# Kernel optimization log

Measured on AMD Instinct MI355X. Metric: run time of the kernel, lower is better.

The kernel has to match this reference:

```python
import jax, jax.numpy as jnp
import numpy as np

B, S, D, H = 4, 2048, 1024, 16
DK = D // H


def setup_inputs() -> dict:
    key = jax.random.key(0)
    ks = jax.random.split(key, 12)
    s = 1.0 / np.sqrt(D)
    return {
        "query": jax.random.normal(ks[0], (B, S, D), jnp.float32),
        "key": jax.random.normal(ks[1], (B, S, D), jnp.float32),
        "value": jax.random.normal(ks[2], (B, S, D), jnp.float32),
        "attention_mask": jax.random.randint(ks[3], (B, S, S), 0, 2, jnp.int32),
        "w_q": jax.random.uniform(ks[4], (D, D), jnp.float32, -s, s),
        "b_q": jax.random.uniform(ks[5], (D,), jnp.float32, -s, s),
        "w_k": jax.random.uniform(ks[6], (D, D), jnp.float32, -s, s),
        "b_k": jax.random.uniform(ks[7], (D,), jnp.float32, -s, s),
        "w_v": jax.random.uniform(ks[8], (D, D), jnp.float32, -s, s),
        "b_v": jax.random.uniform(ks[9], (D,), jnp.float32, -s, s),
        "w_o": jax.random.uniform(ks[10], (D, D), jnp.float32, -s, s),
        "b_o": jax.random.uniform(ks[11], (D,), jnp.float32, -s, s),
    }


def reference(query, key, value, attention_mask, w_q, b_q, w_k, b_k, w_v, b_v, w_o, b_o):
    # project and split heads: [B,S,D] -> [B,H,S,DK]
    def proj(x, w, b):
        y = jnp.einsum('bsd,ed->bse', x, w) + b  # torch Linear: x @ W.T + b
        return y.reshape(B, S, H, DK).transpose(0, 2, 1, 3)

    q = proj(query, w_q, b_q)
    k = proj(key, w_k, b_k)
    v = proj(value, w_v, b_v)

    scores = jnp.einsum('bhqd,bhkd->bhqk', q, k) / np.sqrt(DK).astype(np.float32)
    mask = attention_mask[:, None, :, :]  # broadcast over heads
    scores = jnp.where(mask == 0, jnp.float32(-1e9), scores)
    attn = jax.nn.softmax(scores, axis=-1)  # dropout is identity in eval
    out = jnp.einsum('bhqk,bhkd->bhqd', attn, v)
    out = out.transpose(0, 2, 1, 3).reshape(B, S, D)
    return jnp.einsum('bsd,ed->bse', out, w_o) + b_o
```

## Files before the change

### kernel.cpp

```cpp
#include <hip/hip_runtime.h>


#define B_ 4
#define S_ 2048
#define D_ 1024
#define H_ 16
#define DK_ 64
#define M_ (B_ * S_)

typedef __attribute__((ext_vector_type(4))) float f32x4;
typedef __attribute__((ext_vector_type(8))) short s16x8;
typedef __attribute__((ext_vector_type(8))) unsigned short u16x8;
typedef __attribute__((ext_vector_type(4))) unsigned short u16x4;

__device__ __forceinline__ unsigned short f2bf(float f) {
    union { float f; unsigned int u; } v; v.f = f;
    unsigned int u = v.u;
    return (unsigned short)((u + 0x7FFFu + ((u >> 16) & 1u)) >> 16);
}

__device__ __forceinline__ void gl2lds16(const unsigned short* g, unsigned short* l) {
    __builtin_amdgcn_global_load_lds((const __attribute__((address_space(1))) void*)g,
                                     (__attribute__((address_space(3))) void*)l, 16, 0, 0);
}

__global__ __launch_bounds__(256) void cvt_bf16(const float* __restrict__ x,
                                                unsigned short* __restrict__ y, int n) {
    int i = (blockIdx.x * 256 + threadIdx.x) * 8;
    if (i + 8 <= n) {
        float4 a = *(const float4*)(x + i);
        float4 b = *(const float4*)(x + i + 4);
        u16x8 r;
        r[0] = f2bf(a.x); r[1] = f2bf(a.y); r[2] = f2bf(a.z); r[3] = f2bf(a.w);
        r[4] = f2bf(b.x); r[5] = f2bf(b.y); r[6] = f2bf(b.z); r[7] = f2bf(b.w);
        *(u16x8*)(y + i) = r;
    }
}

__global__ __launch_bounds__(256) void pack_mask(const int* __restrict__ m,
                                                 unsigned long long* __restrict__ pm) {
    int t = blockIdx.x * 256 + threadIdx.x;
    unsigned long long bits = __ballot(m[t] != 0);
    if ((threadIdx.x & 63) == 0) pm[t >> 6] = bits;
}

template <int MODE>
__global__ __launch_bounds__(256) void gemm_bt(const unsigned short* __restrict__ A,
                                               const unsigned short* __restrict__ Bt,
                                               const float* __restrict__ bias,
                                               float scale, void* __restrict__ Y) {
    __shared__ __align__(16) unsigned short As[128 * 64];
    __shared__ __align__(16) unsigned short Bs[128 * 64];
    const int tid = threadIdx.x;
    const int wave = tid >> 6, lane = tid & 63, quad = lane >> 4, l16 = lane & 15;
    const int m0 = blockIdx.x * 128, n0 = blockIdx.y * 128;
    const int rw = (wave & 1) * 64, cw = (wave >> 1) * 64;

    const int srow = tid >> 3, scol = (tid & 7) * 8;
    const unsigned short* ga = A + (size_t)(m0 + srow) * 1024 + scol;
    const unsigned short* gb = Bt + (size_t)(n0 + srow) * 1024 + scol;

    f32x4 acc[4][4];
#pragma unroll
    for (int mi = 0; mi < 4; mi++)
#pragma unroll
        for (int ni = 0; ni < 4; ni++) acc[mi][ni] = (f32x4){0.f, 0.f, 0.f, 0.f};

    for (int k0 = 0; k0 < 1024; k0 += 64) {
#pragma unroll
        for (int r = 0; r < 4; r++) {
            gl2lds16(ga + (size_t)(r * 32) * 1024 + k0, &As[(r * 256 + tid) * 8]);
            gl2lds16(gb + (size_t)(r * 32) * 1024 + k0, &Bs[(r * 256 + tid) * 8]);
        }
        __syncthreads();
#pragma unroll
        for (int kk = 0; kk < 64; kk += 32) {
            s16x8 af[4], bf[4];
#pragma unroll
            for (int mi = 0; mi < 4; mi++)
                af[mi] = *(const s16x8*)&As[(rw + mi * 16 + l16) * 64 + kk + quad * 8];
#pragma unroll
            for (int ni = 0; ni < 4; ni++)
                bf[ni] = *(const s16x8*)&Bs[(cw + ni * 16 + l16) * 64 + kk + quad * 8];
#pragma unroll
            for (int mi = 0; mi < 4; mi++)
#pragma unroll
                for (int ni = 0; ni < 4; ni++)
                    acc[mi][ni] = __builtin_amdgcn_mfma_f32_16x16x32_bf16(af[mi], bf[ni], acc[mi][ni], 0, 0, 0);
        }
        __syncthreads();
    }

    float bv[4];
#pragma unroll
    for (int ni = 0; ni < 4; ni++) bv[ni] = bias[n0 + cw + ni * 16 + l16];
#pragma unroll
    for (int mi = 0; mi < 4; mi++) {
        const int rb = m0 + rw + mi * 16 + quad * 4;
        const int b = rb >> 11, s0 = rb & 2047;
#pragma unroll
        for (int ni = 0; ni < 4; ni++) {
            const int col = n0 + cw + ni * 16 + l16;
            if (MODE == 3) {
#pragma unroll
                for (int i = 0; i < 4; i++)
                    ((float*)Y)[(size_t)(rb + i) * 1024 + col] = (acc[mi][ni][i] + bv[ni]) * scale;
            } else {
                const int h = col >> 6, dk = col & 63;
                if (MODE == 1) {
#pragma unroll
                    for (int i = 0; i < 4; i++)
                        ((unsigned short*)Y)[((size_t)(b * H_ + h) * S_ + s0 + i) * DK_ + dk] =
                            f2bf((acc[mi][ni][i] + bv[ni]) * scale);
                } else {
                    u16x4 pk;
#pragma unroll
                    for (int i = 0; i < 4; i++) pk[i] = f2bf((acc[mi][ni][i] + bv[ni]) * scale);
                    *(u16x4*)&((unsigned short*)Y)[((size_t)(b * H_ + h) * DK_ + dk) * S_ + s0] = pk;
                }
            }
        }
    }
}

__global__ __launch_bounds__(256) void attn_kernel(const unsigned short* __restrict__ Q,
                                                   const unsigned short* __restrict__ K,
                                                   const unsigned short* __restrict__ Vt,
                                                   const unsigned long long* __restrict__ pm,
                                                   unsigned short* __restrict__ ctx) {
    __shared__ __align__(16) unsigned short Ks[64 * 72];
    __shared__ __align__(16) unsigned short Vs[64 * 72];
    __shared__ __align__(16) unsigned short Ps[4 * 16 * 72];

    const int tid = threadIdx.x;
    const int wave = tid >> 6, lane = tid & 63, quad = lane >> 4, l16 = lane & 15;
    const int bh = blockIdx.y, b = bh >> 4, h = bh & 15;
    const int q0 = blockIdx.x * 64;
    const int lr = tid >> 2, lc = (tid & 3) * 16;

    const unsigned short* Kbase = K + (size_t)bh * S_ * DK_;
    const unsigned short* Vbase = Vt + (size_t)bh * DK_ * S_;
    const unsigned long long* pmb = pm + (size_t)b * S_ * 32;

    s16x8 qf0, qf1;
    {
        const unsigned short* qr = Q + ((size_t)bh * S_ + q0 + wave * 16 + l16) * DK_ + quad * 8;
        qf0 = *(const s16x8*)qr;
        qf1 = *(const s16x8*)(qr + 32);
    }

    f32x4 oacc[4];
    float lpart[4];
#pragma unroll
    for (int ct = 0; ct < 4; ct++) oacc[ct] = (f32x4){0.f, 0.f, 0.f, 0.f};
#pragma unroll
    for (int i = 0; i < 4; i++) lpart[i] = 0.f;

    unsigned short* pw = &Ps[wave * 16 * 72];
    const int shl0 = 31 - l16;
    const int shl1 = 15 - l16;

    for (int kt = 0; kt < S_ / 64; kt++) {
        const int k0 = kt * 64;
        const unsigned short* gk = Kbase + (size_t)(k0 + lr) * DK_ + lc;
        const unsigned short* gv = Vbase + (size_t)lr * S_ + k0 + lc;
        *(uint4*)&Ks[lr * 72 + lc] = *(const uint4*)gk;
        *(uint4*)&Ks[lr * 72 + lc + 8] = *(const uint4*)(gk + 8);
        *(uint4*)&Vs[lr * 72 + lc] = *(const uint4*)gv;
        *(uint4*)&Vs[lr * 72 + lc + 8] = *(const uint4*)(gv + 8);
        __syncthreads();

        f32x4 sacc[4];
#pragma unroll
        for (int ct = 0; ct < 4; ct++) sacc[ct] = (f32x4){0.f, 0.f, 0.f, 0.f};
#pragma unroll
        for (int kk = 0; kk < 64; kk += 32) {
            s16x8 af = kk ? qf1 : qf0;
#pragma unroll
            for (int ct = 0; ct < 4; ct++) {
                s16x8 bf = *(const s16x8*)&Ks[(ct * 16 + l16) * 72 + kk + quad * 8];
                sacc[ct] = __builtin_amdgcn_mfma_f32_16x16x32_bf16(af, bf, sacc[ct], 0, 0, 0);
            }
        }

#pragma unroll
        for (int i = 0; i < 4; i++) {
            const int qg = q0 + wave * 16 + quad * 4 + i;
            const uint2 mv = *(const uint2*)&pmb[(size_t)qg * 32 + kt];
#pragma unroll
            for (int ct = 0; ct < 4; ct++) {
                const unsigned mm = (ct & 2) ? mv.y : mv.x;
                const int sh = (ct & 1) ? shl1 : shl0;
                const float sv = ((int)(mm << sh) < 0) ? sacc[ct][i] : -1e30f;
                const float p = exp2f(sv);
                lpart[i] += p;
                pw[(quad * 4 + i) * 72 + ct * 16 + l16] = f2bf(p);
            }
        }

#pragma unroll
        for (int kk = 0; kk < 64; kk += 32) {
            s16x8 af = *(const s16x8*)&pw[l16 * 72 + kk + quad * 8];
#pragma unroll
            for (int ct = 0; ct < 4; ct++) {
                s16x8 bf = *(const s16x8*)&Vs[(ct * 16 + l16) * 72 + kk + quad * 8];
                oacc[ct] = __builtin_amdgcn_mfma_f32_16x16x32_bf16(af, bf, oacc[ct], 0, 0, 0);
            }
        }
        __syncthreads();
    }

    float rl[4];
#pragma unroll
    for (int i = 0; i < 4; i++) {
        float l = lpart[i];
#pragma unroll
        for (int off = 1; off <= 8; off <<= 1) l += __shfl_xor(l, off);
        rl[i] = 1.0f / l;
    }
#pragma unroll
    for (int ct = 0; ct < 4; ct++) {
        const int col = h * DK_ + ct * 16 + l16;
#pragma unroll
        for (int i = 0; i < 4; i++) {
            const int sg = q0 + wave * 16 + quad * 4 + i;
            ctx[((size_t)(b * S_ + sg)) * D_ + col] = f2bf(oacc[ct][i] * rl[i]);
        }
    }
}

extern "C" void kernel_launch(void* const* d_in, const int* in_sizes, int n_in,
                              void* d_out, int out_size, void* d_ws, size_t ws_size,
                              hipStream_t stream) {
    const float* query = (const float*)d_in[0];
    const float* key   = (const float*)d_in[1];
    const float* value = (const float*)d_in[2];
    const int*   mask  = (const int*)d_in[3];
    const float* w_q = (const float*)d_in[4];
    const float* b_q = (const float*)d_in[5];
    const float* w_k = (const float*)d_in[6];
    const float* b_k = (const float*)d_in[7];
    const float* w_v = (const float*)d_in[8];
    const float* b_v = (const float*)d_in[9];
    const float* w_o = (const float*)d_in[10];
    const float* b_o = (const float*)d_in[11];

    char* ws = (char*)d_ws;
    const size_t XSZ = (size_t)M_ * D_ * 2;
    const size_t WSZ = (size_t)D_ * D_ * 2;
    unsigned short* Xq  = (unsigned short*)(ws);
    unsigned short* Xk  = (unsigned short*)(ws + XSZ);
    unsigned short* Xv  = (unsigned short*)(ws + 2 * XSZ);
    unsigned short* Wq  = (unsigned short*)(ws + 3 * XSZ);
    unsigned short* Wk  = (unsigned short*)(ws + 3 * XSZ + WSZ);
    unsigned short* Wv  = (unsigned short*)(ws + 3 * XSZ + 2 * WSZ);
    unsigned short* Wo  = (unsigned short*)(ws + 3 * XSZ + 3 * WSZ);
    unsigned short* Qb  = (unsigned short*)(ws + 3 * XSZ + 4 * WSZ);
    unsigned short* Kb  = (unsigned short*)(ws + 4 * XSZ + 4 * WSZ);
    unsigned short* Vtb = (unsigned short*)(ws + 5 * XSZ + 4 * WSZ);
    unsigned short* ctx = (unsigned short*)(ws + 6 * XSZ + 4 * WSZ);
    unsigned long long* pm = (unsigned long long*)(ws);

    const int nTok = M_ * D_;
    const int nW = D_ * D_;
    hipLaunchKernelGGL(cvt_bf16, dim3(nTok / 2048), dim3(256), 0, stream, query, Xq, nTok);
    hipLaunchKernelGGL(cvt_bf16, dim3(nTok / 2048), dim3(256), 0, stream, key, Xk, nTok);
    hipLaunchKernelGGL(cvt_bf16, dim3(nTok / 2048), dim3(256), 0, stream, value, Xv, nTok);
    hipLaunchKernelGGL(cvt_bf16, dim3(nW / 2048), dim3(256), 0, stream, w_q, Wq, nW);
    hipLaunchKernelGGL(cvt_bf16, dim3(nW / 2048), dim3(256), 0, stream, w_k, Wk, nW);
    hipLaunchKernelGGL(cvt_bf16, dim3(nW / 2048), dim3(256), 0, stream, w_v, Wv, nW);
    hipLaunchKernelGGL(cvt_bf16, dim3(nW / 2048), dim3(256), 0, stream, w_o, Wo, nW);

    const float QSCALE = 0.125f * 1.44269504f;
    dim3 ggrid(M_ / 128, D_ / 128);
    hipLaunchKernelGGL(HIP_KERNEL_NAME(gemm_bt<1>), ggrid, dim3(256), 0, stream, Xq, Wq, b_q, QSCALE, (void*)Qb);
    hipLaunchKernelGGL(HIP_KERNEL_NAME(gemm_bt<1>), ggrid, dim3(256), 0, stream, Xk, Wk, b_k, 1.0f, (void*)Kb);
    hipLaunchKernelGGL(HIP_KERNEL_NAME(gemm_bt<2>), ggrid, dim3(256), 0, stream, Xv, Wv, b_v, 1.0f, (void*)Vtb);

    hipLaunchKernelGGL(pack_mask, dim3((B_ * S_ * S_) / 256), dim3(256), 0, stream, mask, pm);

    hipLaunchKernelGGL(attn_kernel, dim3(S_ / 64, B_ * H_), dim3(256), 0, stream,
                       Qb, Kb, Vtb, pm, ctx);

    hipLaunchKernelGGL(HIP_KERNEL_NAME(gemm_bt<3>), ggrid, dim3(256), 0, stream, ctx, Wo, b_o, 1.0f, d_out);
}
```

Before: 518.4 us.

## Restructure attention kernel: 128-query tiles, transposed S MFMA, direct LDS loads

The attention kernel now handles 128 queries per block, 32 per wave, so each K/V tile staged in LDS is reused across twice as many queries. K and V are loaded straight into LDS with global_load_lds instead of going through registers. The QK product is computed transposed so each lane gets a single query's mask word, masking becomes a bitwise AND, and P is packed to bf16 by truncation. Row sums come from an extra MFMA against a ones vector instead of scalar adds and shuffles. The tradeoffs are more register pressure, a grid with half as many blocks, and unpadded K/V LDS rows that may cause bank conflicts.

```diff
diff --git a/kernel.cpp b/kernel.cpp
--- a/kernel.cpp
+++ b/kernel.cpp
@@ -128,103 +128,129 @@
                                                    const unsigned short* __restrict__ Vt,
                                                    const unsigned long long* __restrict__ pm,
                                                    unsigned short* __restrict__ ctx) {
-    __shared__ __align__(16) unsigned short Ks[64 * 72];
-    __shared__ __align__(16) unsigned short Vs[64 * 72];
-    __shared__ __align__(16) unsigned short Ps[4 * 16 * 72];
+    __shared__ __align__(16) unsigned short Ks[64 * 64];
+    __shared__ __align__(16) unsigned short Vs[64 * 64];
+    __shared__ __align__(16) unsigned short Ps[8 * 16 * 72];
 
     const int tid = threadIdx.x;
     const int wave = tid >> 6, lane = tid & 63, quad = lane >> 4, l16 = lane & 15;
     const int bh = blockIdx.y, b = bh >> 4, h = bh & 15;
-    const int q0 = blockIdx.x * 64;
-    const int lr = tid >> 2, lc = (tid & 3) * 16;
+    const int q0 = blockIdx.x * 128;
+    const int qbase = q0 + wave * 32;
 
     const unsigned short* Kbase = K + (size_t)bh * S_ * DK_;
     const unsigned short* Vbase = Vt + (size_t)bh * DK_ * S_;
     const unsigned long long* pmb = pm + (size_t)b * S_ * 32;
 
-    s16x8 qf0, qf1;
-    {
-        const unsigned short* qr = Q + ((size_t)bh * S_ + q0 + wave * 16 + l16) * DK_ + quad * 8;
-        qf0 = *(const s16x8*)qr;
-        qf1 = *(const s16x8*)(qr + 32);
-    }
-
-    f32x4 oacc[4];
-    float lpart[4];
-#pragma unroll
-    for (int ct = 0; ct < 4; ct++) oacc[ct] = (f32x4){0.f, 0.f, 0.f, 0.f};
-#pragma unroll
-    for (int i = 0; i < 4; i++) lpart[i] = 0.f;
-
-    unsigned short* pw = &Ps[wave * 16 * 72];
-    const int shl0 = 31 - l16;
-    const int shl1 = 15 - l16;
+    s16x8 qf[2][2];
+#pragma unroll
+    for (int qb = 0; qb < 2; qb++) {
+        const unsigned short* qr = Q + ((size_t)bh * S_ + qbase + qb * 16 + l16) * DK_ + quad * 8;
+        qf[qb][0] = *(const s16x8*)qr;
+        qf[qb][1] = *(const s16x8*)(qr + 32);
+    }
+
+    s16x8 ones;
+#pragma unroll
+    for (int j = 0; j < 8; j++) ones[j] = (short)0x3F80;
+
+    f32x4 oacc[2][4], lacc[2];
+#pragma unroll
+    for (int qb = 0; qb < 2; qb++) {
+        lacc[qb] = (f32x4){0.f, 0.f, 0.f, 0.f};
+#pragma unroll
+        for (int ct = 0; ct < 4; ct++) oacc[qb][ct] = (f32x4){0.f, 0.f, 0.f, 0.f};
+    }
+
+    const int q4 = quad * 4;
+    const int stag_r = tid >> 3, stag_c = (tid & 7) * 8;
 
     for (int kt = 0; kt < S_ / 64; kt++) {
         const int k0 = kt * 64;
-        const unsigned short* gk = Kbase + (size_t)(k0 + lr) * DK_ + lc;
-        const unsigned short* gv = Vbase + (size_t)lr * S_ + k0 + lc;
-        *(uint4*)&Ks[lr * 72 + lc] = *(const uint4*)gk;
-        *(uint4*)&Ks[lr * 72 + lc + 8] = *(const uint4*)(gk + 8);
-        *(uint4*)&Vs[lr * 72 + lc] = *(const uint4*)gv;
-        *(uint4*)&Vs[lr * 72 + lc + 8] = *(const uint4*)(gv + 8);
+        gl2lds16(Kbase + (size_t)(k0 + stag_r) * DK_ + stag_c, &Ks[tid * 8]);
+        gl2lds16(Kbase + (size_t)(k0 + 32 + stag_r) * DK_ + stag_c, &Ks[2048 + tid * 8]);
+        gl2lds16(Vbase + (size_t)stag_r * S_ + k0 + stag_c, &Vs[tid * 8]);
+        gl2lds16(Vbase + (size_t)(32 + stag_r) * S_ + k0 + stag_c, &Vs[2048 + tid * 8]);
         __syncthreads();
 
-        f32x4 sacc[4];
-#pragma unroll
-        for (int ct = 0; ct < 4; ct++) sacc[ct] = (f32x4){0.f, 0.f, 0.f, 0.f};
-#pragma unroll
-        for (int kk = 0; kk < 64; kk += 32) {
-            s16x8 af = kk ? qf1 : qf0;
+        f32x4 sacc[2][4];
+#pragma unroll
+        for (int qb = 0; qb < 2; qb++)
+#pragma unroll
+            for (int ct = 0; ct < 4; ct++) sacc[qb][ct] = (f32x4){0.f, 0.f, 0.f, 0.f};
+#pragma unroll
+        for (int kki = 0; kki < 2; kki++) {
+            const int kk = kki * 32;
+            s16x8 kf[4];
+#pragma unroll
+            for (int ct = 0; ct < 4; ct++)
+                kf[ct] = *(const s16x8*)&Ks[(ct * 16 + l16) * 64 + kk + quad * 8];
+#pragma unroll
+            for (int qb = 0; qb < 2; qb++)
+#pragma unroll
+                for (int ct = 0; ct < 4; ct++)
+                    sacc[qb][ct] = __builtin_amdgcn_mfma_f32_16x16x32_bf16(kf[ct], qf[qb][kki], sacc[qb][ct], 0, 0, 0);
+        }
+
+#pragma unroll
+        for (int qb = 0; qb < 2; qb++) {
+            unsigned short* pwq = &Ps[(wave * 2 + qb) * 16 * 72];
+            const int q = qbase + qb * 16 + l16;
+            const uint2 mv = *(const uint2*)&pmb[(size_t)q * 32 + kt];
+            const unsigned mqx = mv.x >> q4;
+            const unsigned mqy = mv.y >> q4;
 #pragma unroll
             for (int ct = 0; ct < 4; ct++) {
-                s16x8 bf = *(const s16x8*)&Ks[(ct * 16 + l16) * 72 + kk + quad * 8];
-                sacc[ct] = __builtin_amdgcn_mfma_f32_16x16x32_bf16(af, bf, sacc[ct], 0, 0, 0);
+                const unsigned mq = (ct & 2) ? mqy : mqx;
+                unsigned pu[4];
+#pragma unroll
+                for (int i = 0; i < 4; i++) {
+                    const int pos = (ct & 1) * 16 + i;
+                    const int mb = ((int)(mq << (31 - pos))) >> 31;
+                    const float p = exp2f(sacc[qb][ct][i]);
+                    pu[i] = __float_as_uint(p) & (unsigned)mb;
+                }
+#pragma unroll
+                for (int t = 0; t < 2; t++) {
+                    const unsigned pk = (pu[2 * t] >> 16) | (pu[2 * t + 1] & 0xFFFF0000u);
+                    *(unsigned*)&pwq[l16 * 72 + ct * 16 + q4 + 2 * t] = pk;
+                }
             }
         }
 
 #pragma unroll
-        for (int i = 0; i < 4; i++) {
-            const int qg = q0 + wave * 16 + quad * 4 + i;
-            const uint2 mv = *(const uint2*)&pmb[(size_t)qg * 32 + kt];
-#pragma unroll
-            for (int ct = 0; ct < 4; ct++) {
-                const unsigned mm = (ct & 2) ? mv.y : mv.x;
-                const int sh = (ct & 1) ? shl1 : shl0;
-                const float sv = ((int)(mm << sh) < 0) ? sacc[ct][i] : -1e30f;
-                const float p = exp2f(sv);
-                lpart[i] += p;
-                pw[(quad * 4 + i) * 72 + ct * 16 + l16] = f2bf(p);
+        for (int kki = 0; kki < 2; kki++) {
+            const int kk = kki * 32;
+            s16x8 vf[4];
+#pragma unroll
+            for (int ct = 0; ct < 4; ct++)
+                vf[ct] = *(const s16x8*)&Vs[(ct * 16 + l16) * 64 + kk + quad * 8];
+#pragma unroll
+            for (int qb = 0; qb < 2; qb++) {
+                const unsigned short* pwq = &Ps[(wave * 2 + qb) * 16 * 72];
+                s16x8 pf = *(const s16x8*)&pwq[l16 * 72 + kk + quad * 8];
+#pragma unroll
+                for (int ct = 0; ct < 4; ct++)
+                    oacc[qb][ct] = __builtin_amdgcn_mfma_f32_16x16x32_bf16(pf, vf[ct], oacc[qb][ct], 0, 0, 0);
+                lacc[qb] = __builtin_amdgcn_mfma_f32_16x16x32_bf16(pf, ones, lacc[qb], 0, 0, 0);
             }
         }
-
-#pragma unroll
-        for (int kk = 0; kk < 64; kk += 32) {
-            s16x8 af = *(const s16x8*)&pw[l16 * 72 + kk + quad * 8];
-#pragma unroll
-            for (int ct = 0; ct < 4; ct++) {
-                s16x8 bf = *(const s16x8*)&Vs[(ct * 16 + l16) * 72 + kk + quad * 8];
-                oacc[ct] = __builtin_amdgcn_mfma_f32_16x16x32_bf16(af, bf, oacc[ct], 0, 0, 0);
+        __syncthreads();
+    }
+
+#pragma unroll
+    for (int qb = 0; qb < 2; qb++) {
+        f32x4 rl;
+#pragma unroll
+        for (int i = 0; i < 4; i++) rl[i] = 1.0f / lacc[qb][i];
+#pragma unroll
+        for (int ct = 0; ct < 4; ct++) {
+            const int col = h * DK_ + ct * 16 + l16;
+#pragma unroll
+            for (int i = 0; i < 4; i++) {
+                const int sg = qbase + qb * 16 + quad * 4 + i;
+                ctx[((size_t)(b * S_ + sg)) * D_ + col] = f2bf(oacc[qb][ct][i] * rl[i]);
             }
-        }
-        __syncthreads();
-    }
-
-    float rl[4];
-#pragma unroll
-    for (int i = 0; i < 4; i++) {
-        float l = lpart[i];
-#pragma unroll
-        for (int off = 1; off <= 8; off <<= 1) l += __shfl_xor(l, off);
-        rl[i] = 1.0f / l;
-    }
-#pragma unroll
-    for (int ct = 0; ct < 4; ct++) {
-        const int col = h * DK_ + ct * 16 + l16;
-#pragma unroll
-        for (int i = 0; i < 4; i++) {
-            const int sg = q0 + wave * 16 + quad * 4 + i;
-            ctx[((size_t)(b * S_ + sg)) * D_ + col] = f2bf(oacc[ct][i] * rl[i]);
         }
     }
 }
@@ -279,7 +305,7 @@
 
     hipLaunchKernelGGL(pack_mask, dim3((B_ * S_ * S_) / 256), dim3(256), 0, stream, mask, pm);
 
-    hipLaunchKernelGGL(attn_kernel, dim3(S_ / 64, B_ * H_), dim3(256), 0, stream,
+    hipLaunchKernelGGL(attn_kernel, dim3(S_ / 128, B_ * H_), dim3(256), 0, stream,
                        Qb, Kb, Vtb, pm, ctx);
 
     hipLaunchKernelGGL(HIP_KERNEL_NAME(gemm_bt<3>), ggrid, dim3(256), 0, stream, ctx, Wo, b_o, 1.0f, d_out);
```

New measurement: 503.4 us. 1.03x faster.
